# Kernel optimization log

Measured on AMD Instinct MI355X. Metric: run time of the kernel, lower is better.

Reference implementation:

```python
import jax, jax.numpy as jnp
import numpy as np
from jax import lax

D_MODEL = 1024
D_INNER = 2048   # expand * d_model
D_STATE = 16
DT_RANK = 64     # ceil(d_model / 16)
D_CONV = 4
B, L = 2, 1024


def setup_inputs() -> dict:
    key = jax.random.key(0)
    ks = jax.random.split(key, 8)
    s = 0.02
    x = jax.random.normal(ks[0], (B, L, D_MODEL), dtype=jnp.float32)
    in_proj_w = jax.random.normal(ks[1], (2 * D_INNER, D_MODEL), dtype=jnp.float32) * s
    conv_w = jax.random.normal(ks[2], (D_INNER, D_CONV), dtype=jnp.float32) * s  # depthwise kernel
    conv_b = jax.random.normal(ks[3], (D_INNER,), dtype=jnp.float32) * s
    x_proj_w = jax.random.normal(ks[4], (DT_RANK + 2 * D_STATE, D_INNER), dtype=jnp.float32) * s
    dt_proj_w = jax.random.normal(ks[5], (D_INNER, DT_RANK), dtype=jnp.float32) * s
    dt_proj_b = jax.random.normal(ks[6], (D_INNER,), dtype=jnp.float32) * s
    A_log = jnp.log(jnp.broadcast_to(jnp.arange(1, D_STATE + 1, dtype=jnp.float32), (D_INNER, D_STATE)))
    D = jnp.ones((D_INNER,), dtype=jnp.float32)
    out_proj_w = jax.random.normal(ks[7], (D_MODEL, D_INNER), dtype=jnp.float32) * s
    return {"x": x, "in_proj_w": in_proj_w, "conv_w": conv_w, "conv_b": conv_b,
            "x_proj_w": x_proj_w, "dt_proj_w": dt_proj_w, "dt_proj_b": dt_proj_b,
            "A_log": A_log, "D": D, "out_proj_w": out_proj_w}


def _causal_depthwise_conv(x, conv_w, conv_b):
    # x: (B, L, d_inner); torch Conv1d(padding=d_conv-1) then [:, :, :L] == causal left pad
    Lx = x.shape[1]
    k = conv_w.shape[-1]
    xp = jnp.pad(x, ((0, 0), (k - 1, 0), (0, 0)))
    out = conv_b
    # small fixed kernel width (4): unrolled taps, fully vectorized over B,L,D
    out = sum(xp[:, i:i + Lx, :] * conv_w[:, i] for i in range(k)) + conv_b
    return out


def mamba_forward(x, in_proj_w, conv_w, conv_b, x_proj_w, dt_proj_w, dt_proj_b, A_log, D, out_proj_w):
    xz = x @ in_proj_w.T                       # (B, L, 2*d_inner)
    xi, z = xz[..., :D_INNER], xz[..., D_INNER:]
    xc = jax.nn.silu(_causal_depthwise_conv(xi, conv_w, conv_b))  # (B, L, d_inner)

    x_dbl = xc @ x_proj_w.T                    # (B, L, dt_rank + 2*d_state)
    dt = x_dbl[..., :DT_RANK]
    Bm = x_dbl[..., DT_RANK:DT_RANK + D_STATE]  # (B, L, N)
    Cm = x_dbl[..., DT_RANK + D_STATE:]         # (B, L, N)
    delta = jax.nn.softplus(dt @ dt_proj_w.T + dt_proj_b)  # (B, L, d_inner)

    A = -jnp.exp(A_log)                        # (d_inner, N)
    deltaA = jnp.exp(delta[..., None] * A)                           # (B, L, D, N)
    deltaBx = delta[..., None] * Bm[:, :, None, :] * xc[..., None]   # (B, L, D, N)

    def step(h, inp):
        dA, dBx, Ct = inp                      # (B,D,N), (B,D,N), (B,N)
        h = dA * h + dBx
        y = jnp.einsum('bdn,bn->bd', h, Ct)
        return h, y

    h0 = jnp.zeros((x.shape[0], D_INNER, D_STATE), dtype=x.dtype)
    _, ys = lax.scan(step, h0, (deltaA.transpose(1, 0, 2, 3),
                                deltaBx.transpose(1, 0, 2, 3),
                                Cm.transpose(1, 0, 2)))
    y = ys.transpose(1, 0, 2)                  # (B, L, d_inner)
    y = y + xc * D
    y = y * jax.nn.silu(z)
    return y @ out_proj_w.T                    # (B, L, d_model)


def reference(x, in_proj_w, conv_w, conv_b, x_proj_w, dt_proj_w, dt_proj_b, A_log, D, out_proj_w):
    return mamba_forward(x, in_proj_w, conv_w, conv_b, x_proj_w, dt_proj_w, dt_proj_b, A_log, D, out_proj_w)
```

## Files before the change

### kernel.cpp

```cpp
#include <hip/hip_runtime.h>
#include <hip/hip_bf16.h>
#include <cstdint>
#include <cstddef>

#define DMODEL 1024
#define DINNER 2048
#define NSTATE 16
#define DTRANK 64
#define BATCH 2
#define SEQ 1024
#define ROWS (BATCH*SEQ)
#define NCHUNK 16
#define CLEN (SEQ/NCHUNK)
#define KSPLIT 16

typedef __attribute__((ext_vector_type(8))) short short8;
typedef __attribute__((ext_vector_type(4))) short short4v;
typedef __attribute__((ext_vector_type(4))) float f32x4;

__device__ __forceinline__ float bf2f(__hip_bfloat16 h){ return __bfloat162float(h); }
__device__ __forceinline__ float sigmoidf_(float x){ return 1.0f/(1.0f + __expf(-x)); }
__device__ __forceinline__ unsigned short f2bfbits(float v){
  __hip_bfloat16 h = __float2bfloat16(v);
  return *(unsigned short*)&h;
}
__device__ __forceinline__ float bfbits2f(unsigned short u){
  unsigned int x = ((unsigned int)u) << 16;
  return *(float*)&x;
}

__device__ __forceinline__ void gld16(const void* g, void* l){
  __builtin_amdgcn_global_load_lds((const __attribute__((address_space(1))) void*)g,
                                   (__attribute__((address_space(3))) void*)l, 16, 0, 0);
}

__global__ void sniff_k(const unsigned short* __restrict__ xu, int* __restrict__ flag)
{
  int t = threadIdx.x;
  int cnt = 0;
  for (int i = t; i < 1024; i += 64) {
    unsigned short u = xu[i];
    int e = (u >> 7) & 0xFF;
    if (e >= 0x70 && e <= 0x86) cnt++;
  }
  for (int o = 32; o; o >>= 1) cnt += __shfl_down(cnt, o);
  if (t == 0) *flag = (cnt >= 768) ? 0 : 1;
}

struct CvtArgs {
  const void *s0,*s1,*s2,*s3,*s4,*s5,*s6,*s7,*s8,*s9;
  __hip_bfloat16 *xB,*inpB,*xprojB,*dtprojB,*outpB;
  float *cwF,*cbF,*dtbF,*alF,*DF;
  float *outZ, *xdblZ;
  const int* flag;
};
#define CVT_C1 2097152
#define CVT_C2 6291456
#define CVT_C3 6299648
#define CVT_C4 6301696
#define CVT_C5 6498304
#define CVT_C6 6629376
#define CVT_C7 6631424
#define CVT_C8 6664192
#define CVT_C9 6666240
#define CVT_TOT 8763392
#define CVT_BLOCKS (CVT_TOT/4/256)

__device__ __forceinline__ void cvt_read4(const void* s, int j, int fl, float v[4]){
  if (fl) {
    f32x4 t = ((const f32x4*)s)[j>>2];
    v[0]=t.x; v[1]=t.y; v[2]=t.z; v[3]=t.w;
  } else {
    short4v t = *(const short4v*)((const __hip_bfloat16*)s + j);
    v[0]=bfbits2f((unsigned short)t.x); v[1]=bfbits2f((unsigned short)t.y);
    v[2]=bfbits2f((unsigned short)t.z); v[3]=bfbits2f((unsigned short)t.w);
  }
}
__device__ __forceinline__ void cvt_wB(__hip_bfloat16* d, int j, const float v[4]){
  short4v o;
  o.x=(short)f2bfbits(v[0]); o.y=(short)f2bfbits(v[1]);
  o.z=(short)f2bfbits(v[2]); o.w=(short)f2bfbits(v[3]);
  *(short4v*)(d + j) = o;
}
__device__ __forceinline__ void cvt_wF(float* d, int j, const float v[4]){
  f32x4 o = { v[0], v[1], v[2], v[3] };
  *(f32x4*)(d + j) = o;
}

__global__ __launch_bounds__(256)
void convert_all_k(CvtArgs a)
{
  int i4 = blockIdx.x * 256 + threadIdx.x;
  const int fl = *a.flag;

  f32x4 z = {0.f, 0.f, 0.f, 0.f};
  if (blockIdx.x < 2048) {
    ((f32x4*)a.outZ)[i4] = z;
  } else if (blockIdx.x < 2048 + 192) {
    ((f32x4*)a.xdblZ)[i4 - 2048*256] = z;
  }

  int i = i4 * 4;
  if (i >= CVT_TOT) return;
  float v[4];
  if (i < CVT_C1)      { cvt_read4(a.s0, i, fl, v);        cvt_wB(a.xB, i, v); }
  else if (i < CVT_C2) { cvt_read4(a.s1, i-CVT_C1, fl, v); cvt_wB(a.inpB, i-CVT_C1, v); }
  else if (i < CVT_C3) { cvt_read4(a.s2, i-CVT_C2, fl, v); cvt_wF(a.cwF, i-CVT_C2, v); }
  else if (i < CVT_C4) { cvt_read4(a.s3, i-CVT_C3, fl, v); cvt_wF(a.cbF, i-CVT_C3, v); }
  else if (i < CVT_C5) { cvt_read4(a.s4, i-CVT_C4, fl, v); cvt_wB(a.xprojB, i-CVT_C4, v); }
  else if (i < CVT_C6) { cvt_read4(a.s5, i-CVT_C5, fl, v); cvt_wB(a.dtprojB, i-CVT_C5, v); }
  else if (i < CVT_C7) { cvt_read4(a.s6, i-CVT_C6, fl, v); cvt_wF(a.dtbF, i-CVT_C6, v); }
  else if (i < CVT_C8) { cvt_read4(a.s7, i-CVT_C7, fl, v); cvt_wF(a.alF, i-CVT_C7, v); }
  else if (i < CVT_C9) { cvt_read4(a.s8, i-CVT_C8, fl, v); cvt_wF(a.DF, i-CVT_C8, v); }
  else                 { cvt_read4(a.s9, i-CVT_C9, fl, v); cvt_wB(a.outpB, i-CVT_C9, v); }
}

template<int EPI>
__global__ __launch_bounds__(256)
void gemm64(const __hip_bfloat16* __restrict__ A,
            const __hip_bfloat16* __restrict__ W,
            int M, int N, int K, int kchunk,
            float* __restrict__ outF,
            __hip_bfloat16* __restrict__ outH,
            __hip_bfloat16* __restrict__ outH2,
            const float* __restrict__ biasF)
{
  __shared__ alignas(16) __hip_bfloat16 As[128*64];
  __shared__ alignas(16) __hip_bfloat16 Ws[128*64];
  const int tid  = threadIdx.x;
  const int lane = tid & 63;
  const int wave = tid >> 6;
  const int wm = wave & 1, wn = wave >> 1;
  const int row0 = blockIdx.y * 128;
  const int col0 = blockIdx.x * 128;

  f32x4 acc[4][4] = {};

  int kbeg = 0, kend = K;
  if (EPI == 5 || EPI == 6) { kbeg = blockIdx.z * kchunk; kend = kbeg + kchunk; }

  const int r16 = lane & 15, q = lane >> 4;
  const int sx0 = ((q ^ (r16 & 7)) * 16);

  for (int k0 = kbeg; k0 < kend; k0 += 64) {
#pragma unroll
    for (int j = 0; j < 4; ++j) {
      int e = tid + j*256;
      int r = e >> 3, g = e & 7;
      int kc = ((g ^ (r & 7)) << 3);
      gld16(A + (size_t)(row0 + r) * K + k0 + kc, (char*)As + (size_t)e*16);
    }
#pragma unroll
    for (int j = 0; j < 4; ++j) {
      int e = tid + j*256;
      int r = e >> 3, g = e & 7;
      int kc = ((g ^ (r & 7)) << 3);
      int rw = col0 + r; if (EPI == 5 && rw > N-1) rw = N-1;
      gld16(W + (size_t)rw * K + k0 + kc, (char*)Ws + (size_t)e*16);
    }
    __syncthreads();

    const char* Ab = (const char*)As + ((wm*64 + r16) * 128);
    const char* Wb = (const char*)Ws + ((wn*64 + r16) * 128);
#pragma unroll
    for (int ksub = 0; ksub < 2; ++ksub) {
      const int sx = sx0 ^ (ksub * 64);
      short8 af[4], wf[4];
#pragma unroll
      for (int i = 0; i < 4; ++i) af[i] = *(const short8*)(Ab + i*16*128 + sx);
#pragma unroll
      for (int i = 0; i < 4; ++i) wf[i] = *(const short8*)(Wb + i*16*128 + sx);
#pragma unroll
      for (int mt = 0; mt < 4; ++mt)
#pragma unroll
        for (int nt = 0; nt < 4; ++nt)
          acc[mt][nt] = __builtin_amdgcn_mfma_f32_16x16x32_bf16(af[mt], wf[nt], acc[mt][nt], 0, 0, 0);
    }
    __syncthreads();
  }

  const int mbase = row0 + wm*64 + (q * 4);
  const int nbase = col0 + wn*64 + r16;

  float bv[4];
  if (EPI == 3) {
#pragma unroll
    for (int nt = 0; nt < 4; ++nt) bv[nt] = biasF[nbase + nt*16];
  }

#pragma unroll
  for (int mt = 0; mt < 4; ++mt) {
#pragma unroll
    for (int nt = 0; nt < 4; ++nt) {
#pragma unroll
      for (int r = 0; r < 4; ++r) {
        int row = mbase + mt*16 + r;
        int col = nbase + nt*16;
        float v = acc[mt][nt][r];
        if (EPI == 3) {
          v += bv[nt];
          float sp = fmaxf(v, 0.0f) + __logf(1.0f + __expf(-fabsf(v)));
          outF[(size_t)row * DINNER + col] = sp;
        } else if (EPI == 4) {
          if (col < DINNER) {
            outH[(size_t)row * DINNER + col] = __float2bfloat16(v);
          } else {
            outH2[(size_t)row * DINNER + (col - DINNER)] = __float2bfloat16(v * sigmoidf_(v));
          }
        } else if (EPI == 5) {
          if (col < 96)
            unsafeAtomicAdd(&outF[(size_t)row * 96 + col], v);
        } else if (EPI == 6) {
          unsafeAtomicAdd(&outF[(size_t)row * DMODEL + col], v);
        }
      }
    }
  }
}

__global__ __launch_bounds__(256)
void dt_cvt_k(const float* __restrict__ xdbl, __hip_bfloat16* __restrict__ dtH)
{
  int i = blockIdx.x * 256 + threadIdx.x;
  if (i >= ROWS*64) return;
  int row = i >> 6, col = i & 63;
  dtH[i] = __float2bfloat16(xdbl[(size_t)row*96 + col]);
}

__global__ __launch_bounds__(256)
void conv_silu_k(const __hip_bfloat16* __restrict__ xi,
                 const float* __restrict__ cw,
                 const float* __restrict__ cb,
                 __hip_bfloat16* __restrict__ xcH)
{
  int idx4 = blockIdx.x * 256 + threadIdx.x;
  int idx  = idx4 * 4;
  int d  = idx & (DINNER - 1);
  int t  = (idx >> 11) & (SEQ - 1);
  int bt = idx >> 11;

  f32x4 cb4 = *(const f32x4*)&cb[d];
  float a0=cb4.x, a1=cb4.y, a2=cb4.z, a3=cb4.w;
  f32x4 w0 = *(const f32x4*)&cw[(d+0)*4];
  f32x4 w1 = *(const f32x4*)&cw[(d+1)*4];
  f32x4 w2 = *(const f32x4*)&cw[(d+2)*4];
  f32x4 w3 = *(const f32x4*)&cw[(d+3)*4];

#pragma unroll
  for (int i = 0; i < 4; ++i) {
    if (t - 3 + i >= 0) {
      short4v xv = *(const short4v*)(xi + (size_t)(bt - 3 + i) * DINNER + d);
      float x0 = bfbits2f((unsigned short)xv.x);
      float x1 = bfbits2f((unsigned short)xv.y);
      float x2 = bfbits2f((unsigned short)xv.z);
      float x3 = bfbits2f((unsigned short)xv.w);
      float c0 = (i==0)?w0.x:(i==1)?w0.y:(i==2)?w0.z:w0.w;
      float c1 = (i==0)?w1.x:(i==1)?w1.y:(i==2)?w1.z:w1.w;
      float c2 = (i==0)?w2.x:(i==1)?w2.y:(i==2)?w2.z:w2.w;
      float c3 = (i==0)?w3.x:(i==1)?w3.y:(i==2)?w3.z:w3.w;
      a0 += c0*x0; a1 += c1*x1; a2 += c2*x2; a3 += c3*x3;
    }
  }
  float y0 = a0 * sigmoidf_(a0);
  float y1 = a1 * sigmoidf_(a1);
  float y2 = a2 * sigmoidf_(a2);
  float y3 = a3 * sigmoidf_(a3);
  short4v o;
  o.x=(short)f2bfbits(y0); o.y=(short)f2bfbits(y1);
  o.z=(short)f2bfbits(y2); o.w=(short)f2bfbits(y3);
  *(short4v*)(xcH + idx) = o;
}

#define GSTEP 8

__global__ __launch_bounds__(256)
void stats_k(const float* __restrict__ delta,
             const __hip_bfloat16* __restrict__ xcH,
             const float* __restrict__ xdbl,
             const float* __restrict__ alF,
             float* __restrict__ Hc, float* __restrict__ Sd)
{
  __shared__ alignas(16) float Bs[CLEN*16];
  const int bid  = blockIdx.x;
  const int b    = bid >> 9;
  const int c    = (bid >> 5) & (NCHUNK-1);
  const int cg   = bid & 31;
  const int tid  = threadIdx.x;
  const int lane = tid & 63;
  const int wave = tid >> 6;
  const int sub  = lane & 3;
  const int ch   = (cg << 6) + (wave << 4) + (lane >> 2);

  const size_t rb = (size_t)b * SEQ + (size_t)c * CLEN;

  for (int i = tid; i < CLEN*16; i += 256) {
    int t = i >> 4, j = i & 15;
    Bs[i] = xdbl[(rb + t)*96 + 64 + j];
  }
  __syncthreads();

  float negA[4];
#pragma unroll
  for (int j = 0; j < 4; ++j) negA[j] = -__expf(alF[ch*NSTATE + sub*4 + j]);

  const float*          dp = delta + rb * DINNER + ch;
  const __hip_bfloat16* xp = xcH   + rb * DINNER + ch;

  float h0=0.f,h1=0.f,h2=0.f,h3=0.f, sd=0.f;
  float d0[GSTEP], x0[GSTEP], d1[GSTEP], x1[GSTEP];

#define PF1(D_,X_,T0) \
  _Pragma("unroll") \
  for (int u = 0; u < GSTEP; ++u) { \
    D_[u] = dp[(size_t)((T0)+u) * DINNER]; \
    X_[u] = bf2f(xp[(size_t)((T0)+u) * DINNER]); \
  }
#define ST1(D_,X_,T0) \
  _Pragma("unroll") \
  for (int u = 0; u < GSTEP; ++u) { \
    float d_ = D_[u]; \
    sd += d_; \
    float du = d_ * X_[u]; \
    f32x4 B4 = *(const f32x4*)&Bs[((T0)+u)*16 + sub*4]; \
    h0 = __expf(d_*negA[0])*h0 + du*B4.x; \
    h1 = __expf(d_*negA[1])*h1 + du*B4.y; \
    h2 = __expf(d_*negA[2])*h2 + du*B4.z; \
    h3 = __expf(d_*negA[3])*h3 + du*B4.w; \
  }

  PF1(d0, x0, 0)
  for (int t0 = 0; t0 < CLEN; t0 += 2*GSTEP) {
    PF1(d1, x1, t0 + GSTEP)
    ST1(d0, x0, t0)
    if (t0 + 2*GSTEP < CLEN) { PF1(d0, x0, t0 + 2*GSTEP) }
    ST1(d1, x1, t0 + GSTEP)
  }
#undef PF1
#undef ST1

  const size_t bc = (size_t)(b*NCHUNK + c);
  f32x4 hv = { h0, h1, h2, h3 };
  *(f32x4*)&Hc[(bc*DINNER + ch)*NSTATE + sub*4] = hv;
  if (sub == 0) Sd[bc*DINNER + ch] = sd;
}

__global__ __launch_bounds__(256)
void carry_k(const float* __restrict__ Hc, const float* __restrict__ Sd,
             const float* __restrict__ alF, float* __restrict__ hin)
{
  int i = blockIdx.x * 256 + threadIdx.x;
  int n  = i & (NSTATE-1);
  int ch = (i >> 4) & (DINNER-1);
  int b  = i >> 15;
  float negA = -__expf(alF[ch * NSTATE + n]);
  float h = 0.f;
#pragma unroll
  for (int c = 0; c < NCHUNK; ++c) {
    size_t bc = (size_t)(b*NCHUNK + c);
    hin[(bc*DINNER + ch)*NSTATE + n] = h;
    float P = __expf(negA * Sd[bc*DINNER + ch]);
    h = P * h + Hc[(bc*DINNER + ch)*NSTATE + n];
  }
}

__global__ __launch_bounds__(256)
void emit_k(const float* __restrict__ delta,
            const __hip_bfloat16* __restrict__ xcH,
            const float* __restrict__ xdbl,
            const __hip_bfloat16* __restrict__ zsH,
            const float* __restrict__ alF,
            const float* __restrict__ DF,
            const float* __restrict__ hin,
            __hip_bfloat16* __restrict__ yH)
{
  __shared__ alignas(16) float BCs[CLEN*32];
  const int bid  = blockIdx.x;
  const int b    = bid >> 9;
  const int c    = (bid >> 5) & (NCHUNK-1);
  const int cg   = bid & 31;
  const int tid  = threadIdx.x;
  const int lane = tid & 63;
  const int wave = tid >> 6;
  const int sub  = lane & 3;
  const int ch   = (cg << 6) + (wave << 4) + (lane >> 2);

  const size_t rb = (size_t)b * SEQ + (size_t)c * CLEN;

  for (int i = tid; i < CLEN*32; i += 256) {
    int t = i >> 5, j = i & 31;
    BCs[i] = xdbl[(rb + t)*96 + 64 + j];
  }
  __syncthreads();

  float negA[4];
#pragma unroll
  for (int j = 0; j < 4; ++j) negA[j] = -__expf(alF[ch*NSTATE + sub*4 + j]);
  const float Dch = DF[ch];

  const float*          dp = delta + rb * DINNER + ch;
  const __hip_bfloat16* xp = xcH   + rb * DINNER + ch;
  const __hip_bfloat16* zp = zsH   + rb * DINNER + ch;
  __hip_bfloat16*       yp = yH    + rb * DINNER + ch;

  f32x4 hv = *(const f32x4*)&hin[((size_t)(b*NCHUNK + c)*DINNER + ch)*NSTATE + sub*4];
  float h0=hv.x, h1=hv.y, h2=hv.z, h3=hv.w;

  float d0[GSTEP], x0[GSTEP], z0[GSTEP], d1[GSTEP], x1[GSTEP], z1[GSTEP];

#define PF(D_,X_,Z_,T0) \
  _Pragma("unroll") \
  for (int u = 0; u < GSTEP; ++u) { \
    D_[u] = dp[(size_t)((T0)+u) * DINNER]; \
    X_[u] = bf2f(xp[(size_t)((T0)+u) * DINNER]); \
    Z_[u] = bf2f(zp[(size_t)((T0)+u) * DINNER]); \
  }
#define STEPS(D_,X_,Z_,T0) \
  _Pragma("unroll") \
  for (int u = 0; u < GSTEP; ++u) { \
    float d_ = D_[u]; \
    float du = d_ * X_[u]; \
    f32x4 B4 = *(const f32x4*)&BCs[((T0)+u)*32 + sub*4]; \
    f32x4 C4 = *(const f32x4*)&BCs[((T0)+u)*32 + 16 + sub*4]; \
    h0 = __expf(d_*negA[0])*h0 + du*B4.x; \
    h1 = __expf(d_*negA[1])*h1 + du*B4.y; \
    h2 = __expf(d_*negA[2])*h2 + du*B4.z; \
    h3 = __expf(d_*negA[3])*h3 + du*B4.w; \
    float p = h0*C4.x + h1*C4.y + h2*C4.z + h3*C4.w; \
    p += __shfl_xor(p, 1); \
    p += __shfl_xor(p, 2); \
    if (sub == 0) { \
      float y = (p + X_[u] * Dch) * Z_[u]; \
      yp[(size_t)((T0)+u) * DINNER] = __float2bfloat16(y); \
    } \
  }

  PF(d0, x0, z0, 0)
  for (int t0 = 0; t0 < CLEN; t0 += 2*GSTEP) {
    PF(d1, x1, z1, t0 + GSTEP)
    STEPS(d0, x0, z0, t0)
    if (t0 + 2*GSTEP < CLEN) { PF(d0, x0, z0, t0 + 2*GSTEP) }
    STEPS(d1, x1, z1, t0 + GSTEP)
  }
#undef PF
#undef STEPS
}

extern "C" void kernel_launch(void* const* d_in, const int* in_sizes, int n_in,
                              void* d_out, int out_size, void* d_ws, size_t ws_size,
                              hipStream_t stream)
{
  float* out = (float*)d_out;
  char* ws = (char*)d_ws;
  const size_t MB = 1024*1024;

  int*            flag    = (int*)            (ws);
  float*          cwF     = (float*)          (ws + 1024);
  float*          cbF     = (float*)          (ws + 40*1024);
  float*          dtbF    = (float*)          (ws + 56*1024);
  float*          alF     = (float*)          (ws + 72*1024);
  float*          DF      = (float*)          (ws + 208*1024);
  float*          Sd      = (float*)          (ws + 256*1024);
  __hip_bfloat16* xB      = (__hip_bfloat16*) (ws + 1*MB);
  __hip_bfloat16* inpB    = (__hip_bfloat16*) (ws + 5*MB);
  __hip_bfloat16* xiB     = (__hip_bfloat16*) (ws + 13*MB);
  float*          dlt     = (float*)          (ws + 1*MB);
  __hip_bfloat16* xprojB  = (__hip_bfloat16*) (ws + 21*MB);
  __hip_bfloat16* dtprojB = (__hip_bfloat16*) (ws + 21*MB + 512*1024);
  __hip_bfloat16* outpB   = (__hip_bfloat16*) (ws + 22*MB);
  __hip_bfloat16* zsH     = (__hip_bfloat16*) (ws + 26*MB);
  __hip_bfloat16* xcH     = (__hip_bfloat16*) (ws + 42*MB);
  float*          xdbl    = (float*)          (ws + 50*MB);
  __hip_bfloat16* dtH     = (__hip_bfloat16*) (ws + 51*MB);
  __hip_bfloat16* yH      = (__hip_bfloat16*) (ws + 52*MB);
  float*          Hc      = (float*)          (ws + 60*MB);
  float*          hin     = (float*)          (ws + 64*MB);

  dim3 blk(256);

  sniff_k<<<1, 64, 0, stream>>>((const unsigned short*)d_in[0], flag);
  CvtArgs ca = { d_in[0], d_in[1], d_in[2], d_in[3], d_in[4],
                 d_in[5], d_in[6], d_in[7], d_in[8], d_in[9],
                 xB, inpB, xprojB, dtprojB, outpB,
                 cwF, cbF, dtbF, alF, DF, out, xdbl, flag };
  convert_all_k<<<CVT_BLOCKS, blk, 0, stream>>>(ca);

  gemm64<4><<<dim3(4096/128, ROWS/128), blk, 0, stream>>>(
      xB, inpB, ROWS, 2*DINNER, DMODEL, 0, nullptr, xiB, zsH, nullptr);

  conv_silu_k<<<(ROWS*DINNER/4)/256, blk, 0, stream>>>(xiB, cwF, cbF, xcH);

  gemm64<5><<<dim3(1, ROWS/128, KSPLIT), blk, 0, stream>>>(
      xcH, xprojB, ROWS, 96, DINNER, DINNER/KSPLIT, xdbl, nullptr, nullptr, nullptr);
  dt_cvt_k<<<(ROWS*64)/256, blk, 0, stream>>>(xdbl, dtH);

  gemm64<3><<<dim3(DINNER/128, ROWS/128), blk, 0, stream>>>(
      dtH, dtprojB, ROWS, DINNER, DTRANK, 0, dlt, nullptr, nullptr, dtbF);

  stats_k<<<BATCH*NCHUNK*32, blk, 0, stream>>>(dlt, xcH, xdbl, alF, Hc, Sd);
  carry_k<<<(BATCH*DINNER*NSTATE)/256, blk, 0, stream>>>(Hc, Sd, alF, hin);
  emit_k<<<BATCH*NCHUNK*32, blk, 0, stream>>>(dlt, xcH, xdbl, zsH, alF, DF, hin, yH);

  gemm64<6><<<dim3(DMODEL/128, ROWS/128, 4), blk, 0, stream>>>(
      yH, outpB, ROWS, DMODEL, DINNER, DINNER/4, out, nullptr, nullptr, nullptr);
}
```

Baseline: 249.3 us.

## Replace out-proj split-K atomics with partial buffers plus reduce; double scan chunks

The output projection's split-K GEMM now writes each K-slice's partial result to its own fp32 buffer instead of atomically adding into the output. A new vectorized kernel sums the four partials into the output, which also removes the need to zero the output in the convert kernel. Separately, the selective-scan chunk count is doubled, giving twice as many stats/emit blocks with shorter chunks and a longer carry pass. This trades atomic contention for extra memory traffic (writing and rereading 4x8MB of partials) and one more launch. Workspace offsets are reshuffled so the partial buffers reuse dead regions.

```diff
diff --git a/kernel.cpp b/kernel.cpp
--- a/kernel.cpp
+++ b/kernel.cpp
@@ -10,7 +10,7 @@
 #define BATCH 2
 #define SEQ 1024
 #define ROWS (BATCH*SEQ)
-#define NCHUNK 16
+#define NCHUNK 32
 #define CLEN (SEQ/NCHUNK)
 #define KSPLIT 16
 
@@ -51,7 +51,7 @@
   const void *s0,*s1,*s2,*s3,*s4,*s5,*s6,*s7,*s8,*s9;
   __hip_bfloat16 *xB,*inpB,*xprojB,*dtprojB,*outpB;
   float *cwF,*cbF,*dtbF,*alF,*DF;
-  float *outZ, *xdblZ;
+  float *xdblZ;
   const int* flag;
 };
 #define CVT_C1 2097152
@@ -93,11 +93,9 @@
   int i4 = blockIdx.x * 256 + threadIdx.x;
   const int fl = *a.flag;
 
-  f32x4 z = {0.f, 0.f, 0.f, 0.f};
-  if (blockIdx.x < 2048) {
-    ((f32x4*)a.outZ)[i4] = z;
-  } else if (blockIdx.x < 2048 + 192) {
-    ((f32x4*)a.xdblZ)[i4 - 2048*256] = z;
+  if (blockIdx.x < 192) {
+    f32x4 z = {0.f, 0.f, 0.f, 0.f};
+    ((f32x4*)a.xdblZ)[i4] = z;
   }
 
   int i = i4 * 4;
@@ -123,7 +121,9 @@
             float* __restrict__ outF,
             __hip_bfloat16* __restrict__ outH,
             __hip_bfloat16* __restrict__ outH2,
-            const float* __restrict__ biasF)
+            const float* __restrict__ biasF,
+            float* __restrict__ q0, float* __restrict__ q1,
+            float* __restrict__ q2, float* __restrict__ q3)
 {
   __shared__ alignas(16) __hip_bfloat16 As[128*64];
   __shared__ alignas(16) __hip_bfloat16 Ws[128*64];
@@ -187,6 +187,9 @@
 #pragma unroll
     for (int nt = 0; nt < 4; ++nt) bv[nt] = biasF[nbase + nt*16];
   }
+  float* qz = nullptr;
+  if (EPI == 6) qz = (blockIdx.z == 0) ? q0 : (blockIdx.z == 1) ? q1
+                   : (blockIdx.z == 2) ? q2 : q3;
 
 #pragma unroll
   for (int mt = 0; mt < 4; ++mt) {
@@ -211,11 +214,27 @@
           if (col < 96)
             unsafeAtomicAdd(&outF[(size_t)row * 96 + col], v);
         } else if (EPI == 6) {
-          unsafeAtomicAdd(&outF[(size_t)row * DMODEL + col], v);
+          qz[(size_t)row * DMODEL + col] = v;
         }
       }
     }
   }
+}
+
+__global__ __launch_bounds__(256)
+void reduce_out_k(const float* __restrict__ q0, const float* __restrict__ q1,
+                  const float* __restrict__ q2, const float* __restrict__ q3,
+                  float* __restrict__ out)
+{
+  int i4 = blockIdx.x * 256 + threadIdx.x;
+  if (i4 >= ROWS*DMODEL/4) return;
+  f32x4 a = ((const f32x4*)q0)[i4];
+  f32x4 b = ((const f32x4*)q1)[i4];
+  f32x4 c = ((const f32x4*)q2)[i4];
+  f32x4 d = ((const f32x4*)q3)[i4];
+  f32x4 o = { (a.x+b.x)+(c.x+d.x), (a.y+b.y)+(c.y+d.y),
+              (a.z+b.z)+(c.z+d.z), (a.w+b.w)+(c.w+d.w) };
+  ((f32x4*)out)[i4] = o;
 }
 
 __global__ __launch_bounds__(256)
@@ -282,7 +301,7 @@
 {
   __shared__ alignas(16) float Bs[CLEN*16];
   const int bid  = blockIdx.x;
-  const int b    = bid >> 9;
+  const int b    = bid >> 10;
   const int c    = (bid >> 5) & (NCHUNK-1);
   const int cg   = bid & 31;
   const int tid  = threadIdx.x;
@@ -375,7 +394,7 @@
 {
   __shared__ alignas(16) float BCs[CLEN*32];
   const int bid  = blockIdx.x;
-  const int b    = bid >> 9;
+  const int b    = bid >> 10;
   const int c    = (bid >> 5) & (NCHUNK-1);
   const int cg   = bid & 31;
   const int tid  = threadIdx.x;
@@ -472,8 +491,12 @@
   float*          xdbl    = (float*)          (ws + 50*MB);
   __hip_bfloat16* dtH     = (__hip_bfloat16*) (ws + 51*MB);
   __hip_bfloat16* yH      = (__hip_bfloat16*) (ws + 52*MB);
-  float*          Hc      = (float*)          (ws + 60*MB);
-  float*          hin     = (float*)          (ws + 64*MB);
+  float*          Hc      = (float*)          (ws + 68*MB);
+  float*          hin     = (float*)          (ws + 76*MB);
+  float*          q0      = (float*)          (ws + 1*MB);
+  float*          q1      = (float*)          (ws + 9*MB);
+  float*          q2      = (float*)          (ws + 26*MB);
+  float*          q3      = (float*)          (ws + 34*MB);
 
   dim3 blk(256);
 
@@ -481,25 +504,30 @@
   CvtArgs ca = { d_in[0], d_in[1], d_in[2], d_in[3], d_in[4],
                  d_in[5], d_in[6], d_in[7], d_in[8], d_in[9],
                  xB, inpB, xprojB, dtprojB, outpB,
-                 cwF, cbF, dtbF, alF, DF, out, xdbl, flag };
+                 cwF, cbF, dtbF, alF, DF, xdbl, flag };
   convert_all_k<<<CVT_BLOCKS, blk, 0, stream>>>(ca);
 
   gemm64<4><<<dim3(4096/128, ROWS/128), blk, 0, stream>>>(
-      xB, inpB, ROWS, 2*DINNER, DMODEL, 0, nullptr, xiB, zsH, nullptr);
+      xB, inpB, ROWS, 2*DINNER, DMODEL, 0, nullptr, xiB, zsH, nullptr,
+      nullptr, nullptr, nullptr, nullptr);
 
   conv_silu_k<<<(ROWS*DINNER/4)/256, blk, 0, stream>>>(xiB, cwF, cbF, xcH);
 
   gemm64<5><<<dim3(1, ROWS/128, KSPLIT), blk, 0, stream>>>(
-      xcH, xprojB, ROWS, 96, DINNER, DINNER/KSPLIT, xdbl, nullptr, nullptr, nullptr);
+      xcH, xprojB, ROWS, 96, DINNER, DINNER/KSPLIT, xdbl, nullptr, nullptr, nullptr,
+      nullptr, nullptr, nullptr, nullptr);
   dt_cvt_k<<<(ROWS*64)/256, blk, 0, stream>>>(xdbl, dtH);
 
   gemm64<3><<<dim3(DINNER/128, ROWS/128), blk, 0, stream>>>(
-      dtH, dtprojB, ROWS, DINNER, DTRANK, 0, dlt, nullptr, nullptr, dtbF);
+      dtH, dtprojB, ROWS, DINNER, DTRANK, 0, dlt, nullptr, nullptr, dtbF,
+      nullptr, nullptr, nullptr, nullptr);
 
   stats_k<<<BATCH*NCHUNK*32, blk, 0, stream>>>(dlt, xcH, xdbl, alF, Hc, Sd);
   carry_k<<<(BATCH*DINNER*NSTATE)/256, blk, 0, stream>>>(Hc, Sd, alF, hin);
   emit_k<<<BATCH*NCHUNK*32, blk, 0, stream>>>(dlt, xcH, xdbl, zsH, alF, DF, hin, yH);
 
   gemm64<6><<<dim3(DMODEL/128, ROWS/128, 4), blk, 0, stream>>>(
-      yH, outpB, ROWS, DMODEL, DINNER, DINNER/4, out, nullptr, nullptr, nullptr);
-}
+      yH, outpB, ROWS, DMODEL, DINNER, DINNER/4, nullptr, nullptr, nullptr, nullptr,
+      q0, q1, q2, q3);
+  reduce_out_k<<<(ROWS*DMODEL/4)/256, blk, 0, stream>>>(q0, q1, q2, q3, out);
+}
```

Measured after the change: 231.8 us. 7.0% less time.
